# Optimization experiments

Hardware: AMD Instinct MI355X
Metric: run time of the kernel (lower is better)

## Reference

```python
import jax, jax.numpy as jnp
import numpy as np

NUM_EXPERTS = 8
TOP_K = 2
HIDDEN = 1024
INTER = 2048
BATCH, SEQ = 2, 2048


def setup_inputs() -> dict:
    key = jax.random.key(0)
    k1, k2, k3, k4 = jax.random.split(key, 4)
    hidden_states = jax.random.normal(k1, (BATCH, SEQ, HIDDEN), dtype=jnp.float32)
    # 0.02 init scale keeps router softmax unsaturated and activations sane
    router_w = jax.random.normal(k2, (NUM_EXPERTS, HIDDEN), dtype=jnp.float32) * 0.02
    up_w = jax.random.normal(k3, (NUM_EXPERTS, HIDDEN, INTER), dtype=jnp.float32) * 0.02
    down_w = jax.random.normal(k4, (NUM_EXPERTS, INTER, HIDDEN), dtype=jnp.float32) * 0.02
    return {"hidden_states": hidden_states, "router_w": router_w, "up_w": up_w, "down_w": down_w}


def reference(hidden_states, router_w, up_w, down_w):
    batch, seq_len, hidden = hidden_states.shape
    flat = hidden_states.reshape(-1, hidden)            # [N, H]
    num_tokens = flat.shape[0]

    router_logits = flat @ router_w.T                   # [N, E]
    router_probs = jax.nn.softmax(router_logits, axis=-1)
    top_weights, top_indices = jax.lax.top_k(router_probs, TOP_K)  # [N, k]
    top_weights = top_weights / jnp.sum(top_weights, axis=-1, keepdims=True)

    # scatter normalized top-k weights into a dense [N, E] mask
    rows = jnp.arange(num_tokens)[:, None]
    expert_mask = jnp.zeros((num_tokens, NUM_EXPERTS), dtype=flat.dtype)
    expert_mask = expert_mask.at[rows, top_indices].set(top_weights)

    # dense path: all experts on all tokens via batched matmul
    h = jnp.einsum('nh,ehf->enf', flat, up_w)           # [E, N, F]
    h = jax.nn.gelu(h, approximate=False)               # torch nn.GELU default = erf
    expert_out = jnp.einsum('enf,efh->enh', h, down_w)  # [E, N, H]
    output = jnp.einsum('enh,ne->nh', expert_out, expert_mask)
    output = output.reshape(batch, seq_len, hidden)

    # load-balancing aux loss; f is computed under no_grad in torch
    one_hot = jnp.zeros((num_tokens, NUM_EXPERTS), dtype=jnp.float32)
    one_hot = one_hot.at[rows, top_indices].set(1.0)
    f = jax.lax.stop_gradient(jnp.sum(one_hot, axis=0) / (num_tokens * TOP_K))
    P = jnp.mean(router_probs, axis=0)
    aux_loss = NUM_EXPERTS * jnp.sum(f * P)
    return output, aux_loss
```

## Files before the change

kernel.cpp:

```cpp
#include <hip/hip_runtime.h>
#include <math.h>

#define NE 8
#define HD 1024
#define FD 2048
#define NT 4096
#define NSLOT (NT * 2)

typedef __attribute__((ext_vector_type(8))) _Float16 half8;
typedef __attribute__((ext_vector_type(4))) float floatx4;

__device__ __forceinline__ void gload_lds(const _Float16* g, _Float16* l) {
  __builtin_amdgcn_global_load_lds(
      (const __attribute__((address_space(1))) unsigned int*)g,
      (__attribute__((address_space(3))) unsigned int*)l, 16, 0, 0);
}

__global__ void transpose_cvt(const float* __restrict__ in, _Float16* __restrict__ outp,
                              int R, int C) {
  __shared__ float t[32][65];
  int e = blockIdx.z;
  int r0 = blockIdx.x * 32, c0 = blockIdx.y * 64;
  int tx = threadIdx.x, ty = threadIdx.y;
  const float* src = in + (size_t)e * R * C;
#pragma unroll
  for (int i = 0; i < 8; i++)
    t[ty + 4 * i][tx] = src[(size_t)(r0 + ty + 4 * i) * C + c0 + tx];
  __syncthreads();
  _Float16* dst = outp + (size_t)e * R * C;
  int tid = ty * 64 + tx;
  int col = tid >> 2, rq = tid & 3;
  union { _Float16 h[8]; uint4 v; } o;
#pragma unroll
  for (int k = 0; k < 8; k++) o.h[k] = (_Float16)t[rq * 8 + k][col];
  *(uint4*)(dst + (size_t)(c0 + col) * R + r0 + rq * 8) = o.v;
}

__global__ __launch_bounds__(256) void router_probs_kernel(
    const float* __restrict__ x, const float* __restrict__ rw, _Float16* __restrict__ xh,
    float* __restrict__ probs, int* __restrict__ sel_e, float* __restrict__ sel_w) {
  int n = blockIdx.x * 4 + (threadIdx.x >> 6);
  int lane = threadIdx.x & 63;
  const float* xr = x + (size_t)n * HD;
  float xv[16];
#pragma unroll
  for (int t = 0; t < 16; t++) xv[t] = xr[lane + 64 * t];
  _Float16* xhr = xh + (size_t)n * HD;
#pragma unroll
  for (int t = 0; t < 16; t++) xhr[lane + 64 * t] = (_Float16)xv[t];
  float logits[NE];
#pragma unroll
  for (int e = 0; e < NE; e++) {
    const float* w = rw + (size_t)e * HD;
    float acc = 0.f;
#pragma unroll
    for (int t = 0; t < 16; t++) acc += xv[t] * w[lane + 64 * t];
    for (int off = 32; off > 0; off >>= 1) acc += __shfl_down(acc, off);
    logits[e] = acc;
  }
  if (lane == 0) {
    float mx = logits[0];
#pragma unroll
    for (int e = 1; e < NE; e++) mx = fmaxf(mx, logits[e]);
    float p[NE]; float s = 0.f;
#pragma unroll
    for (int e = 0; e < NE; e++) { p[e] = expf(logits[e] - mx); s += p[e]; }
    float inv = 1.f / s;
#pragma unroll
    for (int e = 0; e < NE; e++) { p[e] *= inv; probs[n * NE + e] = p[e]; }
    int i1 = 0;
#pragma unroll
    for (int e = 1; e < NE; e++) if (p[e] > p[i1]) i1 = e;
    int i2 = -1; float p2 = -1.f;
#pragma unroll
    for (int e = 0; e < NE; e++) {
      if (e == i1) continue;
      if (p[e] > p2) { p2 = p[e]; i2 = e; }
    }
    float wn = 1.f / (p[i1] + p[i2]);
    sel_e[n * 2 + 0] = i1; sel_w[n * 2 + 0] = p[i1] * wn;
    sel_e[n * 2 + 1] = i2; sel_w[n * 2 + 1] = p[i2] * wn;
  }
}

__global__ __launch_bounds__(1024) void router_reduce_kernel(
    const float* __restrict__ probs, const int* __restrict__ sel_e,
    int* __restrict__ counts, int* __restrict__ offs, int* __restrict__ cursor,
    float* __restrict__ aux_out) {
  int t = threadIdx.x;
  int lane = t & 63, wave = t >> 6;
  float ps[NE];
  int cn[NE];
#pragma unroll
  for (int e = 0; e < NE; e++) { ps[e] = 0.f; cn[e] = 0; }
  for (int r = t; r < NT; r += 1024) {
    const float* pr = probs + (size_t)r * NE;
#pragma unroll
    for (int e = 0; e < NE; e++) ps[e] += pr[e];
  }
  for (int i = t; i < NSLOT; i += 1024) {
    int e = sel_e[i];
#pragma unroll
    for (int j = 0; j < NE; j++) cn[j] += (e == j) ? 1 : 0;
  }
  for (int off = 32; off > 0; off >>= 1) {
#pragma unroll
    for (int e = 0; e < NE; e++) {
      ps[e] += __shfl_down(ps[e], off);
      cn[e] += __shfl_down(cn[e], off);
    }
  }
  __shared__ float sps[16][NE];
  __shared__ int scn[16][NE];
  if (lane == 0) {
#pragma unroll
    for (int e = 0; e < NE; e++) { sps[wave][e] = ps[e]; scn[wave][e] = cn[e]; }
  }
  __syncthreads();
  if (t == 0) {
    float tot_p[NE]; int tot_c[NE];
#pragma unroll
    for (int e = 0; e < NE; e++) { tot_p[e] = 0.f; tot_c[e] = 0; }
    for (int w = 0; w < 16; w++)
#pragma unroll
      for (int e = 0; e < NE; e++) { tot_p[e] += sps[w][e]; tot_c[e] += scn[w][e]; }
    int o = 0;
    float aux = 0.f;
    for (int e = 0; e < NE; e++) {
      counts[e] = tot_c[e];
      offs[e] = o; o += tot_c[e];
      cursor[e] = 0;
      aux += ((float)tot_c[e] / (float)NSLOT) * (tot_p[e] / (float)NT);
    }
    aux_out[0] = (float)NE * aux;
  }
}

__global__ __launch_bounds__(256) void build_gather(
    const int* __restrict__ sel_e, const float* __restrict__ sel_w,
    const int* __restrict__ offs, int* __restrict__ cursor,
    int* __restrict__ gtok, float* __restrict__ gw, int* __restrict__ srow) {
  __shared__ int lh[NE], lbase[NE];
  int t = threadIdx.x;
  int i = blockIdx.x * 256 + t;
  if (t < NE) lh[t] = 0;
  __syncthreads();
  int e = sel_e[i];
  int lrank = atomicAdd(&lh[e], 1);
  __syncthreads();
  if (t < NE) lbase[t] = atomicAdd(&cursor[t], lh[t]);
  __syncthreads();
  int row = offs[e] + lbase[e] + lrank;
  gtok[row] = i >> 1;
  gw[row] = sel_w[i];
  srow[i] = row;
}

template <int KDIM, int NDIM, bool IS_UP>
__global__ __launch_bounds__(256, 2) void moe_gemm2(
    const _Float16* __restrict__ Abase, const _Float16* __restrict__ Bt,
    const int* __restrict__ counts, const int* __restrict__ offs,
    const int* __restrict__ gtok, const float* __restrict__ gw,
    _Float16* __restrict__ Hout, float* __restrict__ Dout) {
  int e = blockIdx.x;
  int cnt = counts[e];
  int m0 = blockIdx.y * 128;
  if (m0 >= cnt) return;
  int n0 = blockIdx.z * 128;
  int off = offs[e];

  __shared__ __align__(16) _Float16 As[2][128 * 64];
  __shared__ __align__(16) _Float16 Bs[2][128 * 64];

  int tid = threadIdx.x;
  int lane = tid & 63, wave = tid >> 6;
  int wm = (wave >> 1) * 64, wn = (wave & 1) * 64;

  int srow8 = lane >> 3;
  int chunk = (lane & 7) ^ srow8;
  const _Float16* ga[4];
  const _Float16* gb[4];
  int sbase = wave * 32 * 64;
#pragma unroll
  for (int j = 0; j < 4; j++) {
    int r = wave * 32 + j * 8 + srow8;
    int am = m0 + r;
    if (am > cnt - 1) am = cnt - 1;
    if (IS_UP) {
      ga[j] = Abase + (size_t)gtok[off + am] * KDIM + chunk * 8;
    } else {
      ga[j] = Abase + (size_t)(off + am) * KDIM + chunk * 8;
    }
    gb[j] = Bt + ((size_t)e * NDIM + n0 + r) * KDIM + chunk * 8;
  }

  floatx4 acc[4][4];
#pragma unroll
  for (int i = 0; i < 4; i++)
#pragma unroll
    for (int j = 0; j < 4; j++) acc[i][j] = (floatx4){0.f, 0.f, 0.f, 0.f};

  int fr = lane & 15, g = lane >> 4;
  int sw0 = ((g) ^ (fr & 7)) * 8;
  int sw1 = ((4 + g) ^ (fr & 7)) * 8;

  auto stage = [&](int buf) {
#pragma unroll
    for (int j = 0; j < 4; j++) gload_lds(ga[j], &As[buf][sbase + j * 512]);
#pragma unroll
    for (int j = 0; j < 4; j++) gload_lds(gb[j], &Bs[buf][sbase + j * 512]);
#pragma unroll
    for (int j = 0; j < 4; j++) { ga[j] += 64; gb[j] += 64; }
  };

  auto compute = [&](int buf) {
    const _Float16* Ab = &As[buf][0];
    const _Float16* Bb = &Bs[buf][0];
    half8 af[4], bfv[4];
#pragma unroll
    for (int t = 0; t < 4; t++) {
      af[t] = *(const half8*)(Ab + (wm + t * 16 + fr) * 64 + sw0);
      bfv[t] = *(const half8*)(Bb + (wn + t * 16 + fr) * 64 + sw0);
    }
#pragma unroll
    for (int i = 0; i < 4; i++)
#pragma unroll
      for (int j = 0; j < 4; j++)
        acc[i][j] = __builtin_amdgcn_mfma_f32_16x16x32_f16(af[i], bfv[j], acc[i][j], 0, 0, 0);
#pragma unroll
    for (int t = 0; t < 4; t++) {
      af[t] = *(const half8*)(Ab + (wm + t * 16 + fr) * 64 + sw1);
      bfv[t] = *(const half8*)(Bb + (wn + t * 16 + fr) * 64 + sw1);
    }
#pragma unroll
    for (int i = 0; i < 4; i++)
#pragma unroll
      for (int j = 0; j < 4; j++)
        acc[i][j] = __builtin_amdgcn_mfma_f32_16x16x32_f16(af[i], bfv[j], acc[i][j], 0, 0, 0);
  };

  constexpr int NK = KDIM / 64;
  stage(0);
  for (int kt = 0; kt < NK - 1; ++kt) {
    int cur = kt & 1;
    stage(cur ^ 1);
    asm volatile("s_waitcnt vmcnt(8)" ::: "memory");
    __builtin_amdgcn_s_barrier();
    compute(cur);
    asm volatile("s_waitcnt lgkmcnt(0)" ::: "memory");
    __builtin_amdgcn_s_barrier();
  }
  asm volatile("s_waitcnt vmcnt(0)" ::: "memory");
  __builtin_amdgcn_s_barrier();
  compute((NK - 1) & 1);

  int cq = (lane >> 4) * 4, cc = lane & 15;
#pragma unroll
  for (int i = 0; i < 4; i++) {
#pragma unroll
    for (int r = 0; r < 4; r++) {
      int m = wm + i * 16 + cq + r;
      if (m0 + m < cnt) {
        if (IS_UP) {
          float w = gw[off + m0 + m];
          _Float16* hrow = Hout + (size_t)(off + m0 + m) * NDIM + n0;
#pragma unroll
          for (int j = 0; j < 4; j++) {
            float v = acc[i][j][r];
            float gl = 0.5f * v * (1.f + erff(v * 0.70710678118f));
            hrow[wn + j * 16 + cc] = (_Float16)(gl * w);
          }
        } else {
          float* orow = Dout + (size_t)(off + m0 + m) * HD + n0;
#pragma unroll
          for (int j = 0; j < 4; j++) orow[wn + j * 16 + cc] = acc[i][j][r];
        }
      }
    }
  }
}

__global__ __launch_bounds__(256) void combine_kernel(
    const float* __restrict__ Dout, const int* __restrict__ srow,
    float* __restrict__ out) {
  int n = blockIdx.x;
  int t = threadIdx.x;
  int r0 = srow[n * 2], r1 = srow[n * 2 + 1];
  float4 a = *(const float4*)(Dout + (size_t)r0 * HD + t * 4);
  float4 b = *(const float4*)(Dout + (size_t)r1 * HD + t * 4);
  float4 c; c.x = a.x + b.x; c.y = a.y + b.y; c.z = a.z + b.z; c.w = a.w + b.w;
  *(float4*)(out + (size_t)n * HD + t * 4) = c;
}

extern "C" void kernel_launch(void* const* d_in, const int* in_sizes, int n_in,
                              void* d_out, int out_size, void* d_ws, size_t ws_size,
                              hipStream_t stream) {
  const float* x = (const float*)d_in[0];
  const float* rw = (const float*)d_in[1];
  const float* up_w = (const float*)d_in[2];
  const float* dn_w = (const float*)d_in[3];
  float* out = (float*)d_out;

  char* ws = (char*)d_ws;
  _Float16* Xh   = (_Float16*)(ws + 0);
  _Float16* Wut  = (_Float16*)(ws + 8388608);
  float*    Dout = (float*)(ws + 0);
  _Float16* Wdt  = (_Float16*)(ws + 41943040);
  _Float16* Hbuf = (_Float16*)(ws + 75497472);
  char* tail = ws + 109051904;
  int*   gtok   = (int*)(tail + 0);
  float* gw     = (float*)(tail + 32768);
  int*   sel_e  = (int*)(tail + 65536);
  float* sel_w  = (float*)(tail + 98304);
  int*   srow   = (int*)(tail + 131072);
  float* probs  = (float*)(tail + 163840);
  int*   counts = (int*)(tail + 294912);
  int*   offs   = (int*)(tail + 294944);
  int*   cursor = (int*)(tail + 294976);

  transpose_cvt<<<dim3(HD / 32, FD / 64, NE), dim3(64, 4), 0, stream>>>(up_w, Wut, HD, FD);
  transpose_cvt<<<dim3(FD / 32, HD / 64, NE), dim3(64, 4), 0, stream>>>(dn_w, Wdt, FD, HD);
  router_probs_kernel<<<NT / 4, 256, 0, stream>>>(x, rw, Xh, probs, sel_e, sel_w);
  router_reduce_kernel<<<1, 1024, 0, stream>>>(probs, sel_e, counts, offs, cursor,
                                               out + (size_t)NT * HD);
  build_gather<<<NSLOT / 256, 256, 0, stream>>>(sel_e, sel_w, offs, cursor, gtok, gw, srow);

  moe_gemm2<HD, FD, true><<<dim3(NE, 32, FD / 128), 256, 0, stream>>>(
      Xh, Wut, counts, offs, gtok, gw, Hbuf, nullptr);
  moe_gemm2<FD, HD, false><<<dim3(NE, 32, HD / 128), 256, 0, stream>>>(
      Hbuf, Wdt, counts, offs, gtok, gw, nullptr, Dout);
  combine_kernel<<<NT, 256, 0, stream>>>(Dout, srow, out);
}
```

Before: 349.3 us.

## Enlarge MoE GEMM tiles to 256 rows with 8 waves per block

The grouped expert GEMM moves from 128x128 tiles with 4 waves to 256-row tiles with 8 waves. The up projection uses 256x256 tiles and the down projection uses 256x128, with the column tile size now a template parameter. Larger tiles raise arithmetic intensity and reuse of the staged weight and activation tiles in LDS, and the vmcnt wait is adjusted to the number of loads per stage. In exchange, LDS use and register pressure per block grow, fewer blocks are launched, and padding waste increases for experts whose token count is not a multiple of 256.

Measured after the change: 385.8 us. 1.1x slower.

```diff
diff --git a/kernel.cpp b/kernel.cpp
--- a/kernel.cpp
+++ b/kernel.cpp
@@ -156,31 +156,38 @@
   srow[i] = row;
 }
 
-template <int KDIM, int NDIM, bool IS_UP>
-__global__ __launch_bounds__(256, 2) void moe_gemm2(
+template <int KDIM, int NDIM, int BN, bool IS_UP>
+__global__ __launch_bounds__(512, 2) void moe_gemm3(
     const _Float16* __restrict__ Abase, const _Float16* __restrict__ Bt,
     const int* __restrict__ counts, const int* __restrict__ offs,
     const int* __restrict__ gtok, const float* __restrict__ gw,
     _Float16* __restrict__ Hout, float* __restrict__ Dout) {
+  constexpr int BM = 256;
+  constexpr int CN = BN / 2;
+  constexpr int NFB = CN / 16;
+  constexpr int NB = BN / 64;
+
   int e = blockIdx.x;
   int cnt = counts[e];
-  int m0 = blockIdx.y * 128;
+  int m0 = blockIdx.y * BM;
   if (m0 >= cnt) return;
-  int n0 = blockIdx.z * 128;
+  int n0 = blockIdx.z * BN;
   int off = offs[e];
 
-  __shared__ __align__(16) _Float16 As[2][128 * 64];
-  __shared__ __align__(16) _Float16 Bs[2][128 * 64];
+  __shared__ __align__(16) _Float16 As[2][BM * 64];
+  __shared__ __align__(16) _Float16 Bs[2][BN * 64];
 
   int tid = threadIdx.x;
   int lane = tid & 63, wave = tid >> 6;
-  int wm = (wave >> 1) * 64, wn = (wave & 1) * 64;
+  int wm = (wave >> 1) * 64;
+  int wn = (wave & 1) * CN;
 
   int srow8 = lane >> 3;
   int chunk = (lane & 7) ^ srow8;
   const _Float16* ga[4];
-  const _Float16* gb[4];
-  int sbase = wave * 32 * 64;
+  const _Float16* gb[NB];
+  int sbaseA = wave * 32 * 64;
+  int sbaseB = wave * (BN / 8) * 64;
 #pragma unroll
   for (int j = 0; j < 4; j++) {
     int r = wave * 32 + j * 8 + srow8;
@@ -191,14 +198,18 @@
     } else {
       ga[j] = Abase + (size_t)(off + am) * KDIM + chunk * 8;
     }
+  }
+#pragma unroll
+  for (int j = 0; j < NB; j++) {
+    int r = wave * (BN / 8) + j * 8 + srow8;
     gb[j] = Bt + ((size_t)e * NDIM + n0 + r) * KDIM + chunk * 8;
   }
 
-  floatx4 acc[4][4];
+  floatx4 acc[4][NFB];
 #pragma unroll
   for (int i = 0; i < 4; i++)
 #pragma unroll
-    for (int j = 0; j < 4; j++) acc[i][j] = (floatx4){0.f, 0.f, 0.f, 0.f};
+    for (int j = 0; j < NFB; j++) acc[i][j] = (floatx4){0.f, 0.f, 0.f, 0.f};
 
   int fr = lane & 15, g = lane >> 4;
   int sw0 = ((g) ^ (fr & 7)) * 8;
@@ -206,36 +217,36 @@
 
   auto stage = [&](int buf) {
 #pragma unroll
-    for (int j = 0; j < 4; j++) gload_lds(ga[j], &As[buf][sbase + j * 512]);
-#pragma unroll
-    for (int j = 0; j < 4; j++) gload_lds(gb[j], &Bs[buf][sbase + j * 512]);
-#pragma unroll
-    for (int j = 0; j < 4; j++) { ga[j] += 64; gb[j] += 64; }
+    for (int j = 0; j < 4; j++) gload_lds(ga[j], &As[buf][sbaseA + j * 512]);
+#pragma unroll
+    for (int j = 0; j < NB; j++) gload_lds(gb[j], &Bs[buf][sbaseB + j * 512]);
+#pragma unroll
+    for (int j = 0; j < 4; j++) ga[j] += 64;
+#pragma unroll
+    for (int j = 0; j < NB; j++) gb[j] += 64;
   };
 
   auto compute = [&](int buf) {
     const _Float16* Ab = &As[buf][0];
     const _Float16* Bb = &Bs[buf][0];
-    half8 af[4], bfv[4];
-#pragma unroll
-    for (int t = 0; t < 4; t++) {
-      af[t] = *(const half8*)(Ab + (wm + t * 16 + fr) * 64 + sw0);
-      bfv[t] = *(const half8*)(Bb + (wn + t * 16 + fr) * 64 + sw0);
-    }
+    half8 af[4], bfv[NFB];
+#pragma unroll
+    for (int t = 0; t < 4; t++) af[t] = *(const half8*)(Ab + (wm + t * 16 + fr) * 64 + sw0);
+#pragma unroll
+    for (int u = 0; u < NFB; u++) bfv[u] = *(const half8*)(Bb + (wn + u * 16 + fr) * 64 + sw0);
 #pragma unroll
     for (int i = 0; i < 4; i++)
 #pragma unroll
-      for (int j = 0; j < 4; j++)
+      for (int j = 0; j < NFB; j++)
         acc[i][j] = __builtin_amdgcn_mfma_f32_16x16x32_f16(af[i], bfv[j], acc[i][j], 0, 0, 0);
 #pragma unroll
-    for (int t = 0; t < 4; t++) {
-      af[t] = *(const half8*)(Ab + (wm + t * 16 + fr) * 64 + sw1);
-      bfv[t] = *(const half8*)(Bb + (wn + t * 16 + fr) * 64 + sw1);
-    }
+    for (int t = 0; t < 4; t++) af[t] = *(const half8*)(Ab + (wm + t * 16 + fr) * 64 + sw1);
+#pragma unroll
+    for (int u = 0; u < NFB; u++) bfv[u] = *(const half8*)(Bb + (wn + u * 16 + fr) * 64 + sw1);
 #pragma unroll
     for (int i = 0; i < 4; i++)
 #pragma unroll
-      for (int j = 0; j < 4; j++)
+      for (int j = 0; j < NFB; j++)
         acc[i][j] = __builtin_amdgcn_mfma_f32_16x16x32_f16(af[i], bfv[j], acc[i][j], 0, 0, 0);
   };
 
@@ -244,7 +255,11 @@
   for (int kt = 0; kt < NK - 1; ++kt) {
     int cur = kt & 1;
     stage(cur ^ 1);
-    asm volatile("s_waitcnt vmcnt(8)" ::: "memory");
+    if constexpr (BN == 256) {
+      asm volatile("s_waitcnt vmcnt(8)" ::: "memory");
+    } else {
+      asm volatile("s_waitcnt vmcnt(6)" ::: "memory");
+    }
     __builtin_amdgcn_s_barrier();
     compute(cur);
     asm volatile("s_waitcnt lgkmcnt(0)" ::: "memory");
@@ -265,15 +280,15 @@
           float w = gw[off + m0 + m];
           _Float16* hrow = Hout + (size_t)(off + m0 + m) * NDIM + n0;
 #pragma unroll
-          for (int j = 0; j < 4; j++) {
+          for (int j = 0; j < NFB; j++) {
             float v = acc[i][j][r];
             float gl = 0.5f * v * (1.f + erff(v * 0.70710678118f));
             hrow[wn + j * 16 + cc] = (_Float16)(gl * w);
           }
         } else {
-          float* orow = Dout + (size_t)(off + m0 + m) * HD + n0;
-#pragma unroll
-          for (int j = 0; j < 4; j++) orow[wn + j * 16 + cc] = acc[i][j][r];
+          float* orow = Dout + (size_t)(off + m0 + m) * NDIM + n0;
+#pragma unroll
+          for (int j = 0; j < NFB; j++) orow[wn + j * 16 + cc] = acc[i][j][r];
         }
       }
     }
@@ -325,9 +340,9 @@
                                                out + (size_t)NT * HD);
   build_gather<<<NSLOT / 256, 256, 0, stream>>>(sel_e, sel_w, offs, cursor, gtok, gw, srow);
 
-  moe_gemm2<HD, FD, true><<<dim3(NE, 32, FD / 128), 256, 0, stream>>>(
+  moe_gemm3<HD, FD, 256, true><<<dim3(NE, 16, FD / 256), 512, 0, stream>>>(
       Xh, Wut, counts, offs, gtok, gw, Hbuf, nullptr);
-  moe_gemm2<FD, HD, false><<<dim3(NE, 32, HD / 128), 256, 0, stream>>>(
+  moe_gemm3<FD, HD, 128, false><<<dim3(NE, 16, HD / 128), 512, 0, stream>>>(
       Hbuf, Wdt, counts, offs, gtok, gw, nullptr, Dout);
   combine_kernel<<<NT, 256, 0, stream>>>(Dout, srow, out);
 }
```
